# Kernel optimization log

Hardware: AMD Instinct MI355X
Metric: run time of the kernel (lower is better)

## Reference

```python
import jax, jax.numpy as jnp
import numpy as np

BETA_PERCENTAGE = 0.3
IN_DIM = 256


def setup_inputs() -> dict:
    key = jax.random.key(0)
    k1, k2, k3, k4, k5 = jax.random.split(key, 5)
    B, C, H, W = 32, IN_DIM, 96, 96
    z_in = jax.random.normal(k1, (B, C, H, W), dtype=jnp.float32)
    # 1x1 conv C -> 1: weight [1, C, 1, 1] stored as vector [C], bias [1]
    # kaiming_normal fan_out for conv with out_ch=1, k=1 -> std = sqrt(2/1)
    phi_w = jax.random.normal(k2, (C,), dtype=jnp.float32) * np.sqrt(2.0)
    phi_b = jnp.zeros((1,), dtype=jnp.float32)
    # Linear C -> C (torch default uniform init scale)
    lim = 1.0 / np.sqrt(C)
    mlp_w = jax.random.uniform(k3, (C, C), minval=-lim, maxval=lim, dtype=jnp.float32)
    mlp_b = jax.random.uniform(k4, (C,), minval=-lim, maxval=lim, dtype=jnp.float32)
    return {"z_in": z_in, "phi_w": phi_w, "phi_b": phi_b, "mlp_w": mlp_w, "mlp_b": mlp_b}


def reference(z_in, phi_w, phi_b, mlp_w, mlp_b):
    B, C, H, W = z_in.shape
    HW = H * W
    beta_rank = int(BETA_PERCENTAGE * HW)  # static from shapes
    z_flat = z_in.reshape(B, C, HW)
    # 1x1 conv (C -> 1) == dot over channel dim, flattened over space: [B, HW]
    x = jnp.einsum('bcs,c->bs', z_flat, phi_w) + phi_b[0]
    # top-k over spatial dim; threshold is the k-th largest value
    topv = jax.lax.top_k(x, beta_rank)[0]            # [B, beta_rank]
    thresh = topv[:, -1]                             # [B]
    mask = (x > thresh[:, None]).astype(z_in.dtype)  # [B, HW]
    # masked global average pool over spatial dim (avg_pool1d with kernel=HW)
    gap = jnp.mean(z_flat * mask[:, None, :], axis=-1)  # [B, C]
    out = gap @ mlp_w.T + mlp_b                          # [B, C]
    return out
```

## Files before the change

### kernel.cpp

```cpp
#include <hip/hip_runtime.h>

constexpr int CDIM  = 256;
constexpr int HWSZ  = 9216;
constexpr int BSZ   = 32;
constexpr int KRANK = 2764;

__global__ __launch_bounds__(128) void k_phi(
    const float* __restrict__ z, const float* __restrict__ phi_w,
    const float* __restrict__ phi_b, float* __restrict__ x)
{
    __shared__ float w[CDIM];
    const int tid = threadIdx.x;
    w[tid]       = phi_w[tid];
    w[tid + 128] = phi_w[tid + 128];
    __syncthreads();

    const int blk = blockIdx.x;
    const int b   = blk / 72;
    const int s   = (blk % 72) * 128 + tid;

    const float* zp = z + (size_t)b * CDIM * HWSZ + s;
    float acc = 0.f;
    #pragma unroll 16
    for (int c = 0; c < CDIM; ++c) {
        acc = fmaf(zp[(size_t)c * HWSZ], w[c], acc);
    }
    x[b * HWSZ + s] = acc + phi_b[0];
}

constexpr int NB       = 4096;
constexpr int CHUNK    = NB / 256;
constexpr int CAND_MAX = 128;

__global__ __launch_bounds__(256) void k_select(
    const float* __restrict__ x, float* __restrict__ thresh)
{
    __shared__ float        vals[HWSZ];
    __shared__ unsigned int hist[NB];
    __shared__ float        s_red[8];
    __shared__ unsigned int s_suffix[256];
    __shared__ float        s_cand[CAND_MAX];
    __shared__ unsigned int s_ccount;
    __shared__ int          s_bin;
    __shared__ unsigned int s_krem, s_cnt;
    __shared__ float        s_out;

    const int b = blockIdx.x, tid = threadIdx.x;
    const float* xb = x + b * HWSZ;

    float vmin = INFINITY, vmax = -INFINITY;
    for (int i = tid; i < HWSZ; i += 256) {
        const float v = xb[i];
        vals[i] = v;
        vmin = fminf(vmin, v);
        vmax = fmaxf(vmax, v);
    }
    for (int off = 32; off; off >>= 1) {
        vmin = fminf(vmin, __shfl_down(vmin, off));
        vmax = fmaxf(vmax, __shfl_down(vmax, off));
    }
    if ((tid & 63) == 0) { s_red[tid >> 6] = vmin; s_red[4 + (tid >> 6)] = vmax; }
    __syncthreads();
    vmin = fminf(fminf(s_red[0], s_red[1]), fminf(s_red[2], s_red[3]));
    vmax = fmaxf(fmaxf(s_red[4], s_red[5]), fmaxf(s_red[6], s_red[7]));

    float lo = vmin;
    float inv_w = 0.f;
    unsigned int krem = KRANK;
    int   pred_on = 0, pred_bin = 0;
    float pred_lo = 0.f, pred_inv = 0.f;
    float range = vmax - vmin;
    float result = vmin;
    int done = (range > 0.f) ? 0 : 1;

    for (int iter = 0; iter < 5 && !done; ++iter) {
        inv_w = (float)NB / range;
        for (int i = tid; i < NB; i += 256) hist[i] = 0u;
        __syncthreads();

        for (int i = tid; i < HWSZ; i += 256) {
            const float v = vals[i];
            if (pred_on) {
                int pi = (int)((v - pred_lo) * pred_inv);
                pi = max(0, min(pi, NB - 1));
                if (pi != pred_bin) continue;
            }
            int idx = (int)((v - lo) * inv_w);
            idx = max(0, min(idx, NB - 1));
            atomicAdd(&hist[idx], 1u);
        }
        __syncthreads();

        unsigned int csum = 0;
        for (int j = 0; j < CHUNK; ++j) csum += hist[tid * CHUNK + j];
        s_suffix[tid] = csum;
        __syncthreads();
        for (int off = 1; off < 256; off <<= 1) {
            const unsigned int add = (tid + off < 256) ? s_suffix[tid + off] : 0u;
            __syncthreads();
            s_suffix[tid] += add;
            __syncthreads();
        }
        const unsigned int sfx  = s_suffix[tid];
        const unsigned int sfx1 = (tid < 255) ? s_suffix[tid + 1] : 0u;
        if (sfx >= krem && sfx1 < krem) {
            unsigned int cum_above = sfx1;
            int binr = tid * CHUNK;
            for (int j = CHUNK - 1; j >= 0; --j) {
                const unsigned int h = hist[tid * CHUNK + j];
                if (cum_above + h >= krem) { binr = tid * CHUNK + j; break; }
                cum_above += h;
            }
            s_bin  = binr;
            s_krem = krem - cum_above;
            s_cnt  = hist[binr];
        }
        __syncthreads();
        const int bin = s_bin;
        const unsigned int cnt = s_cnt;
        krem = s_krem;

        if (cnt <= CAND_MAX) {
            if (tid == 0) s_ccount = 0;
            __syncthreads();
            for (int i = tid; i < HWSZ; i += 256) {
                const float v = vals[i];
                if (pred_on) {
                    int pi = (int)((v - pred_lo) * pred_inv);
                    pi = max(0, min(pi, NB - 1));
                    if (pi != pred_bin) continue;
                }
                int idx = (int)((v - lo) * inv_w);
                idx = max(0, min(idx, NB - 1));
                if (idx == bin) {
                    const unsigned int pos = atomicAdd(&s_ccount, 1u);
                    if (pos < CAND_MAX) s_cand[pos] = v;
                }
            }
            __syncthreads();
            const int n = min(s_ccount, (unsigned int)CAND_MAX);
            if (tid < n) {
                const float v = s_cand[tid];
                int g = 0, e = 0;
                for (int j = 0; j < n; ++j) {
                    const float u = s_cand[j];
                    g += (u > v);
                    e += (u == v);
                }
                if (g < (int)krem && g + e >= (int)krem) s_out = v;
            }
            __syncthreads();
            result = s_out;
            done = 1;
        } else {
            pred_on = 1; pred_bin = bin; pred_lo = lo; pred_inv = inv_w;
            const float w = range / (float)NB;
            lo    = lo + (float)bin * w;
            range = w;
            __syncthreads();
        }
    }

    if (tid == 0) thresh[b] = result;
}

__global__ __launch_bounds__(256) void k_gap(
    const float* __restrict__ z, const float* __restrict__ x,
    const float* __restrict__ thresh, float* __restrict__ gap)
{
    const int c = blockIdx.x, b = (BSZ - 1) - blockIdx.y, tid = threadIdx.x;
    const float th = thresh[b];
    const float* zp = z + ((size_t)b * CDIM + c) * HWSZ;
    const float* xp = x + b * HWSZ;

    float acc = 0.f;
    #pragma unroll
    for (int k = 0; k < 9; ++k) {
        const int s = (tid + k * 256) * 4;
        const float4 v  = *reinterpret_cast<const float4*>(zp + s);
        const float4 xv = *reinterpret_cast<const float4*>(xp + s);
        acc += (xv.x > th) ? v.x : 0.f;
        acc += (xv.y > th) ? v.y : 0.f;
        acc += (xv.z > th) ? v.z : 0.f;
        acc += (xv.w > th) ? v.w : 0.f;
    }

    for (int off = 32; off; off >>= 1) acc += __shfl_down(acc, off);
    __shared__ float r[4];
    if ((tid & 63) == 0) r[tid >> 6] = acc;
    __syncthreads();
    if (tid == 0) gap[b * CDIM + c] = (r[0] + r[1] + r[2] + r[3]) * (1.0f / HWSZ);
}

__global__ __launch_bounds__(256) void k_mlp(
    const float* __restrict__ gap, const float* __restrict__ mlp_w,
    const float* __restrict__ mlp_b, float* __restrict__ out)
{
    const int b = blockIdx.x, i = threadIdx.x;
    __shared__ float g[CDIM];
    g[i] = gap[b * CDIM + i];
    __syncthreads();

    const float* wrow = mlp_w + (size_t)i * CDIM;
    float acc = mlp_b[i];
    #pragma unroll 8
    for (int c = 0; c < CDIM; ++c) acc = fmaf(g[c], wrow[c], acc);
    out[b * CDIM + i] = acc;
}

extern "C" void kernel_launch(void* const* d_in, const int* in_sizes, int n_in,
                              void* d_out, int out_size, void* d_ws, size_t ws_size,
                              hipStream_t stream)
{
    const float* z     = (const float*)d_in[0];
    const float* phi_w = (const float*)d_in[1];
    const float* phi_b = (const float*)d_in[2];
    const float* mlp_w = (const float*)d_in[3];
    const float* mlp_b = (const float*)d_in[4];
    float* out = (float*)d_out;

    float* x      = (float*)d_ws;
    float* thresh = x + BSZ * HWSZ;
    float* gap    = thresh + BSZ;

    k_phi   <<<dim3(BSZ * 72),  128, 0, stream>>>(z, phi_w, phi_b, x);
    k_select<<<dim3(BSZ),       256, 0, stream>>>(x, thresh);
    k_gap   <<<dim3(CDIM, BSZ), 256, 0, stream>>>(z, x, thresh, gap);
    k_mlp   <<<dim3(BSZ),       256, 0, stream>>>(gap, mlp_w, mlp_b, out);
}
```

Baseline: 127.8 us.

## Fuse phi, select and gap into a group-pipelined kernel with last-block selection

```diff
diff --git a/kernel.cpp b/kernel.cpp
--- a/kernel.cpp
+++ b/kernel.cpp
@@ -5,126 +5,95 @@
 constexpr int BSZ   = 32;
 constexpr int KRANK = 2764;
 
-__global__ __launch_bounds__(128) void k_phi(
-    const float* __restrict__ z, const float* __restrict__ phi_w,
-    const float* __restrict__ phi_b, float* __restrict__ x)
-{
-    __shared__ float w[CDIM];
-    const int tid = threadIdx.x;
-    w[tid]       = phi_w[tid];
-    w[tid + 128] = phi_w[tid + 128];
-    __syncthreads();
-
-    const int blk = blockIdx.x;
-    const int b   = blk / 72;
-    const int s   = (blk % 72) * 128 + tid;
-
-    const float* zp = z + (size_t)b * CDIM * HWSZ + s;
-    float acc = 0.f;
-    #pragma unroll 16
-    for (int c = 0; c < CDIM; ++c) {
-        acc = fmaf(zp[(size_t)c * HWSZ], w[c], acc);
-    }
-    x[b * HWSZ + s] = acc + phi_b[0];
-}
+constexpr int GROUP  = 8;
+constexpr int NGRP   = BSZ / GROUP;
+constexpr int SBLK   = 128;
+constexpr int PHI_PB = HWSZ / SBLK;
+constexpr int PHI_PG = PHI_PB * GROUP;
+constexpr int GAP_PG = GROUP * CDIM;
 
 constexpr int NB       = 4096;
 constexpr int CHUNK    = NB / 256;
 constexpr int CAND_MAX = 128;
 
-__global__ __launch_bounds__(256) void k_select(
-    const float* __restrict__ x, float* __restrict__ thresh)
+__global__ __launch_bounds__(256) void k_fused(
+    const float* __restrict__ z, const float* __restrict__ phi_w,
+    const float* __restrict__ phi_b, float* __restrict__ x,
+    float* __restrict__ thresh, float* __restrict__ gout,
+    unsigned int* __restrict__ cnt, int phi_g, int gap_g, int nphi)
 {
-    __shared__ float        vals[HWSZ];
+    const int tid = threadIdx.x;
+
+    __shared__ float        w[CDIM];
+    __shared__ float        part[SBLK];
     __shared__ unsigned int hist[NB];
-    __shared__ float        s_red[8];
     __shared__ unsigned int s_suffix[256];
     __shared__ float        s_cand[CAND_MAX];
+    __shared__ float        s_red[8];
     __shared__ unsigned int s_ccount;
     __shared__ int          s_bin;
     __shared__ unsigned int s_krem, s_cnt;
     __shared__ float        s_out;
-
-    const int b = blockIdx.x, tid = threadIdx.x;
-    const float* xb = x + b * HWSZ;
-
-    float vmin = INFINITY, vmax = -INFINITY;
-    for (int i = tid; i < HWSZ; i += 256) {
-        const float v = xb[i];
-        vals[i] = v;
-        vmin = fminf(vmin, v);
-        vmax = fmaxf(vmax, v);
-    }
-    for (int off = 32; off; off >>= 1) {
-        vmin = fminf(vmin, __shfl_down(vmin, off));
-        vmax = fmaxf(vmax, __shfl_down(vmax, off));
-    }
-    if ((tid & 63) == 0) { s_red[tid >> 6] = vmin; s_red[4 + (tid >> 6)] = vmax; }
-    __syncthreads();
-    vmin = fminf(fminf(s_red[0], s_red[1]), fminf(s_red[2], s_red[3]));
-    vmax = fmaxf(fmaxf(s_red[4], s_red[5]), fmaxf(s_red[6], s_red[7]));
-
-    float lo = vmin;
-    float inv_w = 0.f;
-    unsigned int krem = KRANK;
-    int   pred_on = 0, pred_bin = 0;
-    float pred_lo = 0.f, pred_inv = 0.f;
-    float range = vmax - vmin;
-    float result = vmin;
-    int done = (range > 0.f) ? 0 : 1;
-
-    for (int iter = 0; iter < 5 && !done; ++iter) {
-        inv_w = (float)NB / range;
-        for (int i = tid; i < NB; i += 256) hist[i] = 0u;
-        __syncthreads();
-
+    __shared__ int          s_islast;
+
+    if ((int)blockIdx.x < nphi) {
+        const int p    = blockIdx.x;
+        const int b    = phi_g * GROUP + p / PHI_PB;
+        const int s    = (p % PHI_PB) * SBLK + (tid & (SBLK - 1));
+        const int half = tid >> 7;
+
+        w[tid] = phi_w[tid];
+        __syncthreads();
+
+        const float* zp = z + ((size_t)b * CDIM + half * 128) * HWSZ + s;
+        float acc = 0.f;
+        #pragma unroll 16
+        for (int c = 0; c < 128; ++c)
+            acc = fmaf(zp[(size_t)c * HWSZ], w[half * 128 + c], acc);
+
+        if (half) part[tid & 127] = acc;
+        __syncthreads();
+        if (!half) x[b * HWSZ + s] = acc + part[tid] + phi_b[0];
+
+        __threadfence();
+        __syncthreads();
+        if (tid == 0) s_islast = (atomicAdd(&cnt[b], 1u) == (unsigned)(PHI_PB - 1));
+        __syncthreads();
+        if (!s_islast) return;
+        __threadfence();
+
+        const float* xb = x + b * HWSZ;
+
+        float vmin = INFINITY, vmax = -INFINITY;
         for (int i = tid; i < HWSZ; i += 256) {
-            const float v = vals[i];
-            if (pred_on) {
-                int pi = (int)((v - pred_lo) * pred_inv);
-                pi = max(0, min(pi, NB - 1));
-                if (pi != pred_bin) continue;
-            }
-            int idx = (int)((v - lo) * inv_w);
-            idx = max(0, min(idx, NB - 1));
-            atomicAdd(&hist[idx], 1u);
-        }
-        __syncthreads();
-
-        unsigned int csum = 0;
-        for (int j = 0; j < CHUNK; ++j) csum += hist[tid * CHUNK + j];
-        s_suffix[tid] = csum;
-        __syncthreads();
-        for (int off = 1; off < 256; off <<= 1) {
-            const unsigned int add = (tid + off < 256) ? s_suffix[tid + off] : 0u;
-            __syncthreads();
-            s_suffix[tid] += add;
-            __syncthreads();
-        }
-        const unsigned int sfx  = s_suffix[tid];
-        const unsigned int sfx1 = (tid < 255) ? s_suffix[tid + 1] : 0u;
-        if (sfx >= krem && sfx1 < krem) {
-            unsigned int cum_above = sfx1;
-            int binr = tid * CHUNK;
-            for (int j = CHUNK - 1; j >= 0; --j) {
-                const unsigned int h = hist[tid * CHUNK + j];
-                if (cum_above + h >= krem) { binr = tid * CHUNK + j; break; }
-                cum_above += h;
-            }
-            s_bin  = binr;
-            s_krem = krem - cum_above;
-            s_cnt  = hist[binr];
-        }
-        __syncthreads();
-        const int bin = s_bin;
-        const unsigned int cnt = s_cnt;
-        krem = s_krem;
-
-        if (cnt <= CAND_MAX) {
-            if (tid == 0) s_ccount = 0;
-            __syncthreads();
+            const float v = xb[i];
+            vmin = fminf(vmin, v);
+            vmax = fmaxf(vmax, v);
+        }
+        for (int off = 32; off; off >>= 1) {
+            vmin = fminf(vmin, __shfl_down(vmin, off));
+            vmax = fmaxf(vmax, __shfl_down(vmax, off));
+        }
+        if ((tid & 63) == 0) { s_red[tid >> 6] = vmin; s_red[4 + (tid >> 6)] = vmax; }
+        __syncthreads();
+        vmin = fminf(fminf(s_red[0], s_red[1]), fminf(s_red[2], s_red[3]));
+        vmax = fmaxf(fmaxf(s_red[4], s_red[5]), fmaxf(s_red[6], s_red[7]));
+
+        float lo = vmin, inv_w = 0.f;
+        unsigned int krem = KRANK;
+        int   pred_on = 0, pred_bin = 0;
+        float pred_lo = 0.f, pred_inv = 0.f;
+        float range = vmax - vmin;
+        float result = vmin;
+        int done = (range > 0.f) ? 0 : 1;
+
+        for (int iter = 0; iter < 5 && !done; ++iter) {
+            inv_w = (float)NB / range;
+            for (int i = tid; i < NB; i += 256) hist[i] = 0u;
+            __syncthreads();
+
             for (int i = tid; i < HWSZ; i += 256) {
-                const float v = vals[i];
+                const float v = xb[i];
                 if (pred_on) {
                     int pi = (int)((v - pred_lo) * pred_inv);
                     pi = max(0, min(pi, NB - 1));
@@ -132,73 +101,115 @@
                 }
                 int idx = (int)((v - lo) * inv_w);
                 idx = max(0, min(idx, NB - 1));
-                if (idx == bin) {
-                    const unsigned int pos = atomicAdd(&s_ccount, 1u);
-                    if (pos < CAND_MAX) s_cand[pos] = v;
-                }
-            }
-            __syncthreads();
-            const int n = min(s_ccount, (unsigned int)CAND_MAX);
-            if (tid < n) {
-                const float v = s_cand[tid];
-                int g = 0, e = 0;
-                for (int j = 0; j < n; ++j) {
-                    const float u = s_cand[j];
-                    g += (u > v);
-                    e += (u == v);
-                }
-                if (g < (int)krem && g + e >= (int)krem) s_out = v;
-            }
-            __syncthreads();
-            result = s_out;
-            done = 1;
-        } else {
-            pred_on = 1; pred_bin = bin; pred_lo = lo; pred_inv = inv_w;
-            const float w = range / (float)NB;
-            lo    = lo + (float)bin * w;
-            range = w;
-            __syncthreads();
-        }
+                atomicAdd(&hist[idx], 1u);
+            }
+            __syncthreads();
+
+            unsigned int csum = 0;
+            for (int j = 0; j < CHUNK; ++j) csum += hist[tid * CHUNK + j];
+            s_suffix[tid] = csum;
+            __syncthreads();
+            for (int off = 1; off < 256; off <<= 1) {
+                const unsigned int add = (tid + off < 256) ? s_suffix[tid + off] : 0u;
+                __syncthreads();
+                s_suffix[tid] += add;
+                __syncthreads();
+            }
+            const unsigned int sfx  = s_suffix[tid];
+            const unsigned int sfx1 = (tid < 255) ? s_suffix[tid + 1] : 0u;
+            if (sfx >= krem && sfx1 < krem) {
+                unsigned int cum_above = sfx1;
+                int binr = tid * CHUNK;
+                for (int j = CHUNK - 1; j >= 0; --j) {
+                    const unsigned int h = hist[tid * CHUNK + j];
+                    if (cum_above + h >= krem) { binr = tid * CHUNK + j; break; }
+                    cum_above += h;
+                }
+                s_bin  = binr;
+                s_krem = krem - cum_above;
+                s_cnt  = hist[binr];
+            }
+            __syncthreads();
+            const int bin = s_bin;
+            const unsigned int bc = s_cnt;
+            krem = s_krem;
+
+            if (bc <= CAND_MAX) {
+                if (tid == 0) s_ccount = 0;
+                __syncthreads();
+                for (int i = tid; i < HWSZ; i += 256) {
+                    const float v = xb[i];
+                    if (pred_on) {
+                        int pi = (int)((v - pred_lo) * pred_inv);
+                        pi = max(0, min(pi, NB - 1));
+                        if (pi != pred_bin) continue;
+                    }
+                    int idx = (int)((v - lo) * inv_w);
+                    idx = max(0, min(idx, NB - 1));
+                    if (idx == bin) {
+                        const unsigned int pos = atomicAdd(&s_ccount, 1u);
+                        if (pos < CAND_MAX) s_cand[pos] = v;
+                    }
+                }
+                __syncthreads();
+                const int n = min(s_ccount, (unsigned int)CAND_MAX);
+                if (tid < n) {
+                    const float v = s_cand[tid];
+                    int g = 0, e = 0;
+                    for (int j = 0; j < n; ++j) {
+                        const float u = s_cand[j];
+                        g += (u > v);
+                        e += (u == v);
+                    }
+                    if (g < (int)krem && g + e >= (int)krem) s_out = v;
+                }
+                __syncthreads();
+                result = s_out;
+                done = 1;
+            } else {
+                pred_on = 1; pred_bin = bin; pred_lo = lo; pred_inv = inv_w;
+                const float bw = range / (float)NB;
+                lo    = lo + (float)bin * bw;
+                range = bw;
+                __syncthreads();
+            }
+        }
+        if (tid == 0) thresh[b] = result;
+    } else {
+        const int q = blockIdx.x - nphi;
+        const int b = gap_g * GROUP + (q >> 8);
+        const int c = q & 255;
+        const float th = thresh[b];
+        const float* zp = z + ((size_t)b * CDIM + c) * HWSZ;
+        const float* xp = x + b * HWSZ;
+
+        float acc = 0.f;
+        #pragma unroll
+        for (int k = 0; k < 9; ++k) {
+            const int s = (tid + k * 256) * 4;
+            const float4 v  = *reinterpret_cast<const float4*>(zp + s);
+            const float4 xv = *reinterpret_cast<const float4*>(xp + s);
+            acc += (xv.x > th) ? v.x : 0.f;
+            acc += (xv.y > th) ? v.y : 0.f;
+            acc += (xv.z > th) ? v.z : 0.f;
+            acc += (xv.w > th) ? v.w : 0.f;
+        }
+        for (int off = 32; off; off >>= 1) acc += __shfl_down(acc, off);
+        if ((tid & 63) == 0) s_red[tid >> 6] = acc;
+        __syncthreads();
+        if (tid == 0)
+            gout[b * CDIM + c] =
+                (s_red[0] + s_red[1] + s_red[2] + s_red[3]) * (1.0f / HWSZ);
     }
-
-    if (tid == 0) thresh[b] = result;
 }
 
-__global__ __launch_bounds__(256) void k_gap(
-    const float* __restrict__ z, const float* __restrict__ x,
-    const float* __restrict__ thresh, float* __restrict__ gap)
-{
-    const int c = blockIdx.x, b = (BSZ - 1) - blockIdx.y, tid = threadIdx.x;
-    const float th = thresh[b];
-    const float* zp = z + ((size_t)b * CDIM + c) * HWSZ;
-    const float* xp = x + b * HWSZ;
-
-    float acc = 0.f;
-    #pragma unroll
-    for (int k = 0; k < 9; ++k) {
-        const int s = (tid + k * 256) * 4;
-        const float4 v  = *reinterpret_cast<const float4*>(zp + s);
-        const float4 xv = *reinterpret_cast<const float4*>(xp + s);
-        acc += (xv.x > th) ? v.x : 0.f;
-        acc += (xv.y > th) ? v.y : 0.f;
-        acc += (xv.z > th) ? v.z : 0.f;
-        acc += (xv.w > th) ? v.w : 0.f;
-    }
-
-    for (int off = 32; off; off >>= 1) acc += __shfl_down(acc, off);
-    __shared__ float r[4];
-    if ((tid & 63) == 0) r[tid >> 6] = acc;
-    __syncthreads();
-    if (tid == 0) gap[b * CDIM + c] = (r[0] + r[1] + r[2] + r[3]) * (1.0f / HWSZ);
-}
-
 __global__ __launch_bounds__(256) void k_mlp(
-    const float* __restrict__ gap, const float* __restrict__ mlp_w,
+    const float* __restrict__ gout, const float* __restrict__ mlp_w,
     const float* __restrict__ mlp_b, float* __restrict__ out)
 {
     const int b = blockIdx.x, i = threadIdx.x;
     __shared__ float g[CDIM];
-    g[i] = gap[b * CDIM + i];
+    g[i] = gout[b * CDIM + i];
     __syncthreads();
 
     const float* wrow = mlp_w + (size_t)i * CDIM;
@@ -219,12 +230,18 @@
     const float* mlp_b = (const float*)d_in[4];
     float* out = (float*)d_out;
 
-    float* x      = (float*)d_ws;
-    float* thresh = x + BSZ * HWSZ;
-    float* gap    = thresh + BSZ;
-
-    k_phi   <<<dim3(BSZ * 72),  128, 0, stream>>>(z, phi_w, phi_b, x);
-    k_select<<<dim3(BSZ),       256, 0, stream>>>(x, thresh);
-    k_gap   <<<dim3(CDIM, BSZ), 256, 0, stream>>>(z, x, thresh, gap);
-    k_mlp   <<<dim3(BSZ),       256, 0, stream>>>(gap, mlp_w, mlp_b, out);
+    float*        x      = (float*)d_ws;
+    float*        thresh = x + BSZ * HWSZ;
+    float*        gout   = thresh + BSZ;
+    unsigned int* cnt    = (unsigned int*)(gout + BSZ * CDIM);
+
+    hipMemsetAsync(cnt, 0, BSZ * sizeof(unsigned int), stream);
+
+    for (int g = 0; g <= NGRP; ++g) {
+        const int nphi = (g < NGRP) ? PHI_PG : 0;
+        const int ngap = (g > 0)    ? GAP_PG : 0;
+        k_fused<<<dim3(nphi + ngap), 256, 0, stream>>>(
+            z, phi_w, phi_b, x, thresh, gout, cnt, g, g - 1, nphi);
+    }
+    k_mlp<<<dim3(BSZ), 256, 0, stream>>>(gout, mlp_w, mlp_b, out);
 }
```

Measured after the change: 510.6 us. 4x slower.
